# Kernel optimization log

Measured on AMD Instinct MI355X. Metric: run time of the kernel, lower is better.

The kernel has to match this reference:

```python
import jax, jax.numpy as jnp
import numpy as np

N, E, MUL = 50000, 400000, 32
SQ3 = float(np.sqrt(3.0))


def setup_inputs() -> dict:
    key = jax.random.key(0)
    ks = jax.random.split(key, 16)
    rn = lambda k, s: jax.random.normal(k, s, dtype=jnp.float32)
    return {
        "x": rn(ks[0], (N, 4 * MUL)),                       # 32x0e + 32x1o
        "node_attr": jnp.ones((N, 1), jnp.float32),          # 1x0e
        "edge_src": jax.random.randint(ks[1], (E,), 0, N),
        "edge_dst": jax.random.randint(ks[2], (E,), 0, N),
        "edge_sh": rn(ks[3], (E, 4)),                        # SH(lmax=1): 0e + 1o
        "edge_scalars": jax.random.uniform(ks[4], (E, 10), dtype=jnp.float32),
        "W_fc1": rn(ks[5], (10, 100)),
        "W_fc2": rn(ks[6], (100, 4 * MUL)),
        "W_sc0": rn(ks[7], (MUL, MUL)),
        "W_sc1": rn(ks[8], (MUL, MUL)),
        "W_l1_0": rn(ks[9], (MUL, MUL)),
        "W_l1_1": rn(ks[10], (MUL, MUL)),
        "W_l2_0": rn(ks[11], (2 * MUL, MUL)),
        "W_l2_1": rn(ks[12], (2 * MUL, MUL)),
        "W_alpha": rn(ks[13], (2 * MUL, 1)),
    }


def reference(x, node_attr, edge_src, edge_dst, edge_sh, edge_scalars,
              W_fc1, W_fc2, W_sc0, W_sc1, W_l1_0, W_l1_1, W_l2_0, W_l2_1, W_alpha):
    n = x.shape[0]
    x0 = x[:, :MUL]                       # [N, 32]  scalars (0e)
    x1 = x[:, MUL:].reshape(n, MUL, 3)    # [N, 32, 3] vectors (1o)
    a = node_attr                          # [N, 1]
    inv = 1.0 / np.sqrt(MUL)
    inv2 = 1.0 / np.sqrt(2 * MUL)

    # self-connection FCTP(x, attr) -> out irreps (attr is scalar -> per-l linear)
    sc0 = (x0 @ W_sc0) * inv * a
    sc1 = jnp.einsum('nuc,uv->nvc', x1, W_sc1) * inv * a[:, :, None]
    sc = jnp.concatenate([sc0, sc1.reshape(n, 3 * MUL)], axis=1)

    # lin1
    y0 = (x0 @ W_l1_0) * inv * a
    y1 = jnp.einsum('nuc,uv->nvc', x1, W_l1_1) * inv * a[:, :, None]

    # radial MLP -> per-edge tensor-product weights (4 uvu paths x MUL)
    h = jax.nn.silu(edge_scalars @ W_fc1 / np.sqrt(10.0))
    w = (h @ W_fc2) / np.sqrt(100.0)      # [E, 4*MUL]
    w00, w11 = w[:, :MUL], w[:, MUL:2 * MUL]
    w01, w10 = w[:, 2 * MUL:3 * MUL], w[:, 3 * MUL:]

    # gather at source nodes
    x0e = y0[edge_src]                    # [E, 32]
    x1e = y1[edge_src]                    # [E, 32, 3]
    sh0 = edge_sh[:, :1]                  # [E, 1]
    sh1 = edge_sh[:, 1:4]                 # [E, 3]

    # CG-structured 'uvu' paths
    m00 = w00 * x0e * sh0                                           # 0e x 0e -> 0e
    m11 = w11 * jnp.einsum('euc,ec->eu', x1e, sh1) / SQ3            # 1o x 1o -> 0e
    m01 = w01[:, :, None] * x0e[:, :, None] * sh1[:, None, :]       # 0e x 1o -> 1o
    m10 = w10[:, :, None] * x1e * sh0[:, :, None]                   # 1o x 0e -> 1o
    edge_feat = jnp.concatenate(
        [m00, m11, m01.reshape(-1, 3 * MUL), m10.reshape(-1, 3 * MUL)], axis=1)  # [E, 256]

    # scatter-mean to destination nodes
    sums = jax.ops.segment_sum(edge_feat, edge_dst, num_segments=n)
    cnt = jax.ops.segment_sum(jnp.ones((edge_feat.shape[0],), x.dtype), edge_dst, num_segments=n)
    mean = sums / jnp.maximum(cnt, 1.0)[:, None]                    # [N, 256]

    mid0 = mean[:, :2 * MUL]                                        # 64x0e
    mid1 = mean[:, 2 * MUL:].reshape(n, 2 * MUL, 3)                 # 64x1o

    alpha = (mid0 @ W_alpha) * inv2 * a                             # [N, 1]
    c0 = (mid0 @ W_l2_0) * inv2 * a
    c1 = jnp.einsum('nuc,uv->nvc', mid1, W_l2_1) * inv2 * a[:, :, None]
    conv = jnp.concatenate([c0, c1.reshape(n, 3 * MUL)], axis=1)

    # output mask of sc is all ones here -> alpha gating as in source
    return sc + alpha * conv
```

## Files before the change

kernel.cpp:

```cpp
#include <hip/hip_runtime.h>
#include <hip/hip_bf16.h>

#define MUL 32
#define SCAN_CH 1024

typedef _Float16 f16x8 __attribute__((ext_vector_type(8)));
typedef float f32x4 __attribute__((ext_vector_type(4)));

static __device__ __forceinline__ float silu_f(float z) {
    return z / (1.0f + __expf(-z));
}

__global__ __launch_bounds__(256) void node_pre_kernel(
    const float* __restrict__ x, const float* __restrict__ attr,
    const float* __restrict__ Wsc0, const float* __restrict__ Wsc1,
    const float* __restrict__ Wl10, const float* __restrict__ Wl11,
    float* __restrict__ sc_out, _Float16* __restrict__ y_out, int N)
{
    __shared__ float sX[4][128];
    const int tid = threadIdx.x;
    const int wid = tid >> 6, L = tid & 63;
    float* xs = sX[wid];
    const float inv = 0.17677669529663687f;

    const bool t0 = (L < 32);
    const int i1 = t0 ? 0 : (L - 32);
    const int v1 = i1 / 3, c1 = i1 - v1 * 3;
    const int i2 = L + 32;
    const int v2 = i2 / 3, c2 = i2 - v2 * 3;

    const int xb1 = t0 ? 0 : (32 + c1);
    const int xst1 = t0 ? 1 : 3;

    float wA[32], wB[32], wC[32], wD[32];
#pragma unroll
    for (int u = 0; u < 32; ++u) {
        wA[u] = t0 ? Wsc0[u * 32 + L] : Wsc1[u * 32 + v1];
        wB[u] = t0 ? Wl10[u * 32 + L] : Wl11[u * 32 + v1];
        wC[u] = Wsc1[u * 32 + v2];
        wD[u] = Wl11[u * 32 + v2];
    }

    const int stride = gridDim.x * 4;
    for (int n = blockIdx.x * 4 + wid; n < N; n += stride) {
        xs[L]      = x[(size_t)n * 128 + L];
        xs[64 + L] = x[(size_t)n * 128 + 64 + L];
        const float scale = inv * attr[n];
        float a0 = 0.f, a1 = 0.f, b0 = 0.f, b1 = 0.f;
#pragma unroll
        for (int u = 0; u < 32; ++u) {
            const float xv1 = xs[xb1 + u * xst1];
            const float xv2 = xs[32 + u * 3 + c2];
            a0 += xv1 * wA[u];
            a1 += xv1 * wB[u];
            b0 += xv2 * wC[u];
            b1 += xv2 * wD[u];
        }
        sc_out[(size_t)n * 128 + L]      = a0 * scale;
        sc_out[(size_t)n * 128 + 64 + L] = b0 * scale;
        y_out [(size_t)n * 128 + L]      = (_Float16)(a1 * scale);
        y_out [(size_t)n * 128 + 64 + L] = (_Float16)(b1 * scale);
    }
}

__global__ void hist_kernel(const int* __restrict__ edst, int* __restrict__ deg, int E)
{
    int i = blockIdx.x * blockDim.x + threadIdx.x;
    const int stride = gridDim.x * blockDim.x;
    for (; i < E; i += stride) atomicAdd(&deg[edst[i]], 1);
}

__global__ __launch_bounds__(256) void scanA_kernel(
    const int* __restrict__ deg, int* __restrict__ bsum, int N)
{
    __shared__ int red[256];
    const int t = threadIdx.x, b = blockIdx.x;
    const int base = b * SCAN_CH;
    int s = 0;
#pragma unroll
    for (int k = 0; k < 4; ++k) {
        const int idx = base + t + k * 256;
        if (idx < N) s += deg[idx];
    }
    red[t] = s;
    __syncthreads();
    for (int off = 128; off; off >>= 1) {
        if (t < off) red[t] += red[t + off];
        __syncthreads();
    }
    if (t == 0) bsum[b] = red[0];
}

__global__ __launch_bounds__(256) void scanB_kernel(
    const int* __restrict__ bsum, int* __restrict__ boff, int NB)
{
    __shared__ int s[256];
    const int t = threadIdx.x;
    const int v = (t < NB) ? bsum[t] : 0;
    s[t] = v;
    __syncthreads();
    for (int off = 1; off < 256; off <<= 1) {
        const int add = (t >= off) ? s[t - off] : 0;
        __syncthreads();
        s[t] += add;
        __syncthreads();
    }
    if (t < NB) boff[t] = s[t] - v;
}

__global__ __launch_bounds__(256) void scanC_kernel(
    const int* __restrict__ deg, const int* __restrict__ boff,
    int* __restrict__ row_ptr, int N)
{
    __shared__ int ts[256];
    const int t = threadIdx.x, b = blockIdx.x;
    const int base = b * SCAN_CH + t * 4;
    int d0 = 0, d1 = 0, d2 = 0, d3 = 0;
    if (base + 0 < N) d0 = deg[base + 0];
    if (base + 1 < N) d1 = deg[base + 1];
    if (base + 2 < N) d2 = deg[base + 2];
    if (base + 3 < N) d3 = deg[base + 3];
    const int tsum = d0 + d1 + d2 + d3;
    ts[t] = tsum;
    __syncthreads();
    for (int off = 1; off < 256; off <<= 1) {
        const int add = (t >= off) ? ts[t - off] : 0;
        __syncthreads();
        ts[t] += add;
        __syncthreads();
    }
    int run = boff[b] + ts[t] - tsum;
    if (base + 0 <= N) row_ptr[base + 0] = run;
    run += d0;
    if (base + 1 <= N) row_ptr[base + 1] = run;
    run += d1;
    if (base + 2 <= N) row_ptr[base + 2] = run;
    run += d2;
    if (base + 3 <= N) row_ptr[base + 3] = run;
}

__global__ void fill_kernel(
    const int* __restrict__ esrc, const int* __restrict__ edst,
    const float* __restrict__ esh,
    const int* __restrict__ row_ptr, int* __restrict__ cur,
    int* __restrict__ csr2edge, int* __restrict__ src_s, float4* __restrict__ sh_s,
    int E)
{
    int i = blockIdx.x * blockDim.x + threadIdx.x;
    const int stride = gridDim.x * blockDim.x;
    for (; i < E; i += stride) {
        const int d = edst[i];
        const int p = row_ptr[d] + atomicAdd(&cur[d], 1);
        csr2edge[p] = i;
        src_s[p] = esrc[i];
        sh_s[p] = *(const float4*)&esh[(size_t)i * 4];
    }
}

__global__ __launch_bounds__(512) void edge_w_kernel(
    const float* __restrict__ escal, const int* __restrict__ csr2edge,
    const float* __restrict__ Wfc1, const float* __restrict__ Wfc2,
    _Float16* __restrict__ w_s, int E)
{
    __shared__ _Float16 sW2T[128 * 128];
    __shared__ _Float16 sH[8][16 * 128];

    const int tid = threadIdx.x;
    const int wid = tid >> 6;
    const int l   = tid & 63;
    const int c16 = l & 15;
    const int kq  = l >> 4;

    _Float16* Hw = sH[wid];

    {
        int* z2 = (int*)sW2T;
        for (int i = tid; i < 128 * 128 / 2; i += 512) z2[i] = 0;
    }
    __syncthreads();
    for (int i = tid; i < 100 * 128; i += 512) {
        const int k = i >> 7, col = i & 127;
        sW2T[col * 128 + (k ^ ((col & 7) << 3))] = (_Float16)Wfc2[i];
    }

    f16x8 bW1[7];
#pragma unroll
    for (int cb = 0; cb < 7; ++cb) {
        const int col = cb * 16 + c16;
#pragma unroll
        for (int j = 0; j < 8; ++j) {
            const int k = kq * 8 + j;
            bW1[cb][j] = (k < 10 && col < 100) ? (_Float16)Wfc1[k * 100 + col]
                                               : (_Float16)0.f;
        }
    }
#pragma unroll
    for (int r = 0; r < 4; ++r) {
        const int row = kq * 4 + r;
        const int col = 112 + c16;
        Hw[row * 128 + (col ^ ((row & 7) << 3))] = (_Float16)0.f;
    }
    __syncthreads();

    const float inv_s10 = 0.31622776601683794f;

    const int gw = blockIdx.x * 8 + wid;
    const int nw = gridDim.x * 8;
    const int step = nw * 16;

    int base = gw * 16;
    f16x8 a1;
    {
        const int ge = base + c16;
        const int ee = (ge < E) ? csr2edge[ge] : 0;
#pragma unroll
        for (int j = 0; j < 8; ++j) {
            const int k = kq * 8 + j;
            a1[j] = (k < 10 && ge < E) ? (_Float16)escal[(size_t)ee * 10 + k]
                                       : (_Float16)0.f;
        }
    }

    for (; base < E; base += step) {
#pragma unroll
        for (int cb = 0; cb < 7; ++cb) {
            f32x4 z = {0.f, 0.f, 0.f, 0.f};
            z = __builtin_amdgcn_mfma_f32_16x16x32_f16(a1, bW1[cb], z, 0, 0, 0);
#pragma unroll
            for (int r = 0; r < 4; ++r) {
                const int row = kq * 4 + r;
                const int col = cb * 16 + c16;
                const float h = silu_f(z[r] * inv_s10) * 0.1f;
                Hw[row * 128 + (col ^ ((row & 7) << 3))] = (_Float16)h;
            }
        }

        f16x8 a1n;
        {
            const int ge = base + step + c16;
            const int ee = (ge < E) ? csr2edge[ge] : 0;
#pragma unroll
            for (int j = 0; j < 8; ++j) {
                const int k = kq * 8 + j;
                a1n[j] = (k < 10 && ge < E)
                         ? (_Float16)escal[(size_t)ee * 10 + k]
                         : (_Float16)0.f;
            }
        }

        f32x4 acc0 = {0.f,0.f,0.f,0.f}, acc1 = {0.f,0.f,0.f,0.f};
        f32x4 acc2 = {0.f,0.f,0.f,0.f}, acc3 = {0.f,0.f,0.f,0.f};
        f32x4 acc4 = {0.f,0.f,0.f,0.f}, acc5 = {0.f,0.f,0.f,0.f};
        f32x4 acc6 = {0.f,0.f,0.f,0.f}, acc7 = {0.f,0.f,0.f,0.f};
#pragma unroll
        for (int kk = 0; kk < 4; ++kk) {
            const f16x8 a2 = *(const f16x8*)&Hw[c16 * 128 +
                                ((kk * 32 + kq * 8) ^ ((c16 & 7) << 3))];
#define BFRAG(CB) (*(const f16x8*)&sW2T[((CB) * 16 + c16) * 128 + \
                       ((kk * 32 + kq * 8) ^ ((c16 & 7) << 3))])
            acc0 = __builtin_amdgcn_mfma_f32_16x16x32_f16(a2, BFRAG(0), acc0, 0, 0, 0);
            acc1 = __builtin_amdgcn_mfma_f32_16x16x32_f16(a2, BFRAG(1), acc1, 0, 0, 0);
            acc2 = __builtin_amdgcn_mfma_f32_16x16x32_f16(a2, BFRAG(2), acc2, 0, 0, 0);
            acc3 = __builtin_amdgcn_mfma_f32_16x16x32_f16(a2, BFRAG(3), acc3, 0, 0, 0);
            acc4 = __builtin_amdgcn_mfma_f32_16x16x32_f16(a2, BFRAG(4), acc4, 0, 0, 0);
            acc5 = __builtin_amdgcn_mfma_f32_16x16x32_f16(a2, BFRAG(5), acc5, 0, 0, 0);
            acc6 = __builtin_amdgcn_mfma_f32_16x16x32_f16(a2, BFRAG(6), acc6, 0, 0, 0);
            acc7 = __builtin_amdgcn_mfma_f32_16x16x32_f16(a2, BFRAG(7), acc7, 0, 0, 0);
#undef BFRAG
        }

#define STAGE_CB(CB, ACC)                                                     \
        {                                                                     \
            _Pragma("unroll")                                                 \
            for (int r = 0; r < 4; ++r) {                                     \
                const int row = kq * 4 + r;                                   \
                const int col = (CB) * 16 + c16;                              \
                Hw[row * 128 + (col ^ ((row & 7) << 3))] = (_Float16)(ACC)[r];\
            }                                                                 \
        }
        STAGE_CB(0, acc0) STAGE_CB(1, acc1) STAGE_CB(2, acc2) STAGE_CB(3, acc3)
        STAGE_CB(4, acc4) STAGE_CB(5, acc5) STAGE_CB(6, acc6) STAGE_CB(7, acc7)
#undef STAGE_CB

#pragma unroll
        for (int i = 0; i < 4; ++i) {
            const int e = i * 4 + (l >> 4);
            const int colb = (l & 15) * 8;
            const f16x8 v = *(const f16x8*)&Hw[e * 128 +
                                (colb ^ ((e & 7) << 3))];
            if (base + e < E)
                *(f16x8*)&w_s[(size_t)(base + e) * 128 + colb] = v;
        }

        a1 = a1n;
    }
}

__global__ __launch_bounds__(256) void gather_post_kernel(
    const _Float16* __restrict__ w_s, const int* __restrict__ src_s,
    const float4* __restrict__ sh_s, const int* __restrict__ row_ptr,
    const _Float16* __restrict__ y, const float* __restrict__ attr,
    const float* __restrict__ Wl20, const float* __restrict__ Wl21,
    const float* __restrict__ Walpha,
    float* __restrict__ out, int N)
{
    __shared__ float sW0[64 * 32];
    __shared__ float sW1[64 * 32];
    __shared__ float sWa[64];
    __shared__ float sMid[4][256];

    const int tid = threadIdx.x;
    for (int i = tid; i < 64 * 32; i += 256) {
        sW0[i] = Wl20[i];
        sW1[i] = Wl21[i];
    }
    if (tid < 64) sWa[tid] = Walpha[tid];
    __syncthreads();

    const int wid = tid >> 6;
    const int L   = tid & 63;
    const bool hi = (L >= 32);
    const int u   = L & 31;

    const int wAi = hi ? 32 + u : u;
    const int wBi = hi ? 96 + u : 64 + u;
    const int yi0 = hi ? 32 + 3 * u + 0 : u;
    const int yi1 = hi ? 32 + 3 * u + 1 : u;
    const int yi2 = hi ? 32 + 3 * u + 2 : u;
    const float mulA = hi ? 0.5773502691896258f : 1.0f;

    const int o1m = L - 32;
    const int v1 = hi ? o1m / 3 : 0;
    const int c1 = hi ? o1m - v1 * 3 : 0;
    const int o2m = L + 32;
    const int v2 = o2m / 3;
    const int c2 = o2m - v2 * 3;
    const float* wcol1 = hi ? (sW1 + v1) : (sW0 + L);
    const float* wcol2 = sW1 + v2;

    float* midw = &sMid[wid][0];
    const float* msrc1c = hi ? (midw + 64 + c1 * 64) : midw;
    const float* msrc2c = midw + 64 + c2 * 64;

#define ACC_EDGE(sh, wAv, wBv, q0, q1, q2) do {                        \
        const float sA0 = hi ? (sh).y : (sh).x;                        \
        const float sA1 = hi ? (sh).z : 0.f;                           \
        const float sA2 = hi ? (sh).w : 0.f;                           \
        const float b1s = hi ? (sh).x : (sh).y;                        \
        const float b2s = hi ? (sh).x : (sh).z;                        \
        const float b3s = hi ? (sh).x : (sh).w;                        \
        accA += (wAv) * mulA * ((q0) * sA0 + (q1) * sA1 + (q2) * sA2); \
        acc1 += (wBv) * (q0) * b1s;                                    \
        acc2 += (wBv) * (q1) * b2s;                                    \
        acc3 += (wBv) * (q2) * b3s;                                    \
    } while (0)

    const int waves_glob = gridDim.x * 4;
    for (int n = blockIdx.x * 4 + wid; n < N; n += waves_glob) {
        const int jlo = row_ptr[n];
        const int jhi = row_ptr[n + 1];
        const int deg = jhi - jlo;
        if (deg <= 0) continue;

        float accA = 0.f, acc1 = 0.f, acc2 = 0.f, acc3 = 0.f;

        int j = jlo;
        for (; j + 2 <= jhi; j += 2) {
            const int sa = src_s[j];
            const int sb = src_s[j + 1];
            const float4 shA = sh_s[j];
            const float4 shB = sh_s[j + 1];
            const _Float16* wra = w_s + (size_t)j * 128;
            const _Float16* wrb = wra + 128;
            const _Float16* yra = y + (size_t)sa * 128;
            const _Float16* yrb = y + (size_t)sb * 128;
            const float wAa = (float)wra[wAi], wBa = (float)wra[wBi];
            const float qa0 = (float)yra[yi0], qa1 = (float)yra[yi1], qa2 = (float)yra[yi2];
            const float wAb = (float)wrb[wAi], wBb = (float)wrb[wBi];
            const float qb0 = (float)yrb[yi0], qb1 = (float)yrb[yi1], qb2 = (float)yrb[yi2];
            ACC_EDGE(shA, wAa, wBa, qa0, qa1, qa2);
            ACC_EDGE(shB, wAb, wBb, qb0, qb1, qb2);
        }
        if (j < jhi) {
            const int sa = src_s[j];
            const float4 shA = sh_s[j];
            const _Float16* wra = w_s + (size_t)j * 128;
            const _Float16* yra = y + (size_t)sa * 128;
            const float wAa = (float)wra[wAi], wBa = (float)wra[wBi];
            const float qa0 = (float)yra[yi0], qa1 = (float)yra[yi1], qa2 = (float)yra[yi2];
            ACC_EDGE(shA, wAa, wBa, qa0, qa1, qa2);
        }

        const float rdeg = 1.0f / (float)deg;
        const float a = attr[n];

        float term = accA * rdeg * sWa[L];
#pragma unroll
        for (int off = 32; off; off >>= 1) term += __shfl_xor(term, off);
        const float alpha = term * 0.125f * a;

        midw[L]            = accA * rdeg;
        midw[64 + L]       = acc1 * rdeg;
        midw[128 + L]      = acc2 * rdeg;
        midw[192 + L]      = acc3 * rdeg;

        float cv1 = 0.f, cv2 = 0.f;
#pragma unroll
        for (int kk = 0; kk < 16; ++kk) {
            const float4 m1 = *(const float4*)&msrc1c[4 * kk];
            const float4 m2 = *(const float4*)&msrc2c[4 * kk];
            cv1 += m1.x * wcol1[(4 * kk + 0) * 32] + m1.y * wcol1[(4 * kk + 1) * 32]
                 + m1.z * wcol1[(4 * kk + 2) * 32] + m1.w * wcol1[(4 * kk + 3) * 32];
            cv2 += m2.x * wcol2[(4 * kk + 0) * 32] + m2.y * wcol2[(4 * kk + 1) * 32]
                 + m2.z * wcol2[(4 * kk + 2) * 32] + m2.w * wcol2[(4 * kk + 3) * 32];
        }
        const float f = alpha * 0.125f * a;
        const size_t ob = (size_t)n * 128;
        out[ob + L]      += f * cv1;
        out[ob + 64 + L] += f * cv2;
    }
#undef ACC_EDGE
}

extern "C" void kernel_launch(void* const* d_in, const int* in_sizes, int n_in,
                              void* d_out, int out_size, void* d_ws, size_t ws_size,
                              hipStream_t stream)
{
    const float* x      = (const float*)d_in[0];
    const float* attr   = (const float*)d_in[1];
    const int*   esrc   = (const int*)  d_in[2];
    const int*   edst   = (const int*)  d_in[3];
    const float* esh    = (const float*)d_in[4];
    const float* escal  = (const float*)d_in[5];
    const float* Wfc1   = (const float*)d_in[6];
    const float* Wfc2   = (const float*)d_in[7];
    const float* Wsc0   = (const float*)d_in[8];
    const float* Wsc1   = (const float*)d_in[9];
    const float* Wl10   = (const float*)d_in[10];
    const float* Wl11   = (const float*)d_in[11];
    const float* Wl20   = (const float*)d_in[12];
    const float* Wl21   = (const float*)d_in[13];
    const float* Walpha = (const float*)d_in[14];

    const int N = in_sizes[1];
    const int E = in_sizes[2];
    float* out = (float*)d_out;

    char* p = (char*)d_ws;
    _Float16* y   = (_Float16*)p; p += (size_t)N * 128 * sizeof(_Float16);
    int* row_ptr  = (int*)p;      p += (size_t)(N + 1) * sizeof(int);
    int* deg      = (int*)p;      p += (size_t)N * sizeof(int);
    int* cur      = (int*)p;      p += (size_t)N * sizeof(int);
    int* bsum     = (int*)p;      p += 256 * sizeof(int);
    int* boff     = (int*)p;      p += 256 * sizeof(int);
    int* csr2edge = (int*)p;      p += (size_t)E * sizeof(int);
    int* src_s    = (int*)p;      p += (size_t)E * sizeof(int);
    p = (char*)(((uintptr_t)p + 15) & ~(uintptr_t)15);
    float4* sh_s  = (float4*)p;   p += (size_t)E * sizeof(float4);
    _Float16* w_s = (_Float16*)p;

    const int NB = (N + SCAN_CH) / SCAN_CH;

    hipMemsetAsync(deg, 0, (size_t)2 * N * sizeof(int), stream);

    node_pre_kernel<<<1024, 256, 0, stream>>>(x, attr, Wsc0, Wsc1, Wl10, Wl11,
                                              out, y, N);
    hist_kernel<<<512, 256, 0, stream>>>(edst, deg, E);
    scanA_kernel<<<NB, 256, 0, stream>>>(deg, bsum, N);
    scanB_kernel<<<1, 256, 0, stream>>>(bsum, boff, NB);
    scanC_kernel<<<NB, 256, 0, stream>>>(deg, boff, row_ptr, N);
    fill_kernel<<<512, 256, 0, stream>>>(esrc, edst, esh, row_ptr, cur,
                                         csr2edge, src_s, sh_s, E);
    edge_w_kernel<<<512, 512, 0, stream>>>(escal, csr2edge, Wfc1, Wfc2, w_s, E);
    gather_post_kernel<<<4096, 256, 0, stream>>>(w_s, src_s, sh_s, row_ptr,
                                                 y, attr, Wl20, Wl21, Walpha,
                                                 out, N);
}
```

Measured before the change: 243.2 us.

## Fuse radial MLP edge weights with per-node gather-aggregation in one kernel

The edge-weight kernel now partitions the destination-sorted CSR edge range into contiguous per-wave spans aligned to node boundaries, found by binary search on row_ptr. Right after computing each 16-edge tile of tensor-product weights with MFMA, it consumes them from LDS to accumulate the message for each destination node. This removes the round trip of the per-edge weight array (E×128 fp16) through global memory. A small node_post kernel then reads a new fp16 per-node mean buffer and applies the output linears and alpha gating. In exchange, each wave walks its edges one at a time with dependent gathers of y, which reduces memory-level parallelism. The per-node means are also rounded to fp16.

```diff
diff --git a/kernel.cpp b/kernel.cpp
--- a/kernel.cpp
+++ b/kernel.cpp
@@ -9,6 +9,16 @@
 
 static __device__ __forceinline__ float silu_f(float z) {
     return z / (1.0f + __expf(-z));
+}
+
+static __device__ __forceinline__ int lbound(const int* __restrict__ rp,
+                                             int cnt, int target) {
+    int lo = 0, hi = cnt;
+    while (lo < hi) {
+        const int mid = (lo + hi) >> 1;
+        if (rp[mid] < target) lo = mid + 1; else hi = mid;
+    }
+    return lo;
 }
 
 __global__ __launch_bounds__(256) void node_pre_kernel(
@@ -157,10 +167,12 @@
     }
 }
 
-__global__ __launch_bounds__(512) void edge_w_kernel(
+__global__ __launch_bounds__(512) void edge_fused_kernel(
     const float* __restrict__ escal, const int* __restrict__ csr2edge,
     const float* __restrict__ Wfc1, const float* __restrict__ Wfc2,
-    _Float16* __restrict__ w_s, int E)
+    const int* __restrict__ src_s, const float4* __restrict__ sh_s,
+    const int* __restrict__ row_ptr, const _Float16* __restrict__ y,
+    _Float16* __restrict__ mid_g, int N, int E)
 {
     __shared__ _Float16 sW2T[128 * 128];
     __shared__ _Float16 sH[8][16 * 128];
@@ -203,25 +215,47 @@
     __syncthreads();
 
     const float inv_s10 = 0.31622776601683794f;
-
-    const int gw = blockIdx.x * 8 + wid;
-    const int nw = gridDim.x * 8;
-    const int step = nw * 16;
-
-    int base = gw * 16;
+    const float inv_s3  = 0.5773502691896258f;
+
+    const bool hi = (l >= 32);
+    const int u = l & 31;
+    const int wAi = hi ? 32 + u : u;
+    const int wBi = hi ? 96 + u : 64 + u;
+    const int yi0 = hi ? 32 + 3 * u + 0 : u;
+    const int yi1 = hi ? 32 + 3 * u + 1 : u;
+    const int yi2 = hi ? 32 + 3 * u + 2 : u;
+    const float mulA = hi ? inv_s3 : 1.0f;
+
+    const int W = gridDim.x * 8;
+    const int k_w = blockIdx.x * 8 + wid;
+    const int tgt0 = (int)((long)k_w * E / W);
+    const int tgt1 = (int)((long)(k_w + 1) * E / W);
+    const int nlo = lbound(row_ptr, N + 1, tgt0);
+    const int nhi = lbound(row_ptr, N + 1, tgt1);
+    if (nlo >= nhi) return;
+    const int jstart = row_ptr[nlo];
+    const int jend   = row_ptr[nhi];
+    if (jstart >= jend) return;
+
+    int n = nlo;
+    while (n < nhi && row_ptr[n + 1] == row_ptr[n]) ++n;
+    int jhi_n = row_ptr[n + 1];
+
+    float accA = 0.f, ac1 = 0.f, ac2 = 0.f, ac3 = 0.f;
+
     f16x8 a1;
     {
-        const int ge = base + c16;
-        const int ee = (ge < E) ? csr2edge[ge] : 0;
+        const int ge = jstart + c16;
+        const int ee = (ge < jend) ? csr2edge[ge] : 0;
 #pragma unroll
         for (int j = 0; j < 8; ++j) {
             const int k = kq * 8 + j;
-            a1[j] = (k < 10 && ge < E) ? (_Float16)escal[(size_t)ee * 10 + k]
-                                       : (_Float16)0.f;
-        }
-    }
-
-    for (; base < E; base += step) {
+            a1[j] = (k < 10 && ge < jend)
+                    ? (_Float16)escal[(size_t)ee * 10 + k] : (_Float16)0.f;
+        }
+    }
+
+    for (int bb = jstart; bb < jend; bb += 16) {
 #pragma unroll
         for (int cb = 0; cb < 7; ++cb) {
             f32x4 z = {0.f, 0.f, 0.f, 0.f};
@@ -237,35 +271,34 @@
 
         f16x8 a1n;
         {
-            const int ge = base + step + c16;
-            const int ee = (ge < E) ? csr2edge[ge] : 0;
+            const int ge = bb + 16 + c16;
+            const int ee = (ge < jend) ? csr2edge[ge] : 0;
 #pragma unroll
             for (int j = 0; j < 8; ++j) {
                 const int k = kq * 8 + j;
-                a1n[j] = (k < 10 && ge < E)
-                         ? (_Float16)escal[(size_t)ee * 10 + k]
-                         : (_Float16)0.f;
+                a1n[j] = (k < 10 && ge < jend)
+                         ? (_Float16)escal[(size_t)ee * 10 + k] : (_Float16)0.f;
             }
         }
 
-        f32x4 acc0 = {0.f,0.f,0.f,0.f}, acc1 = {0.f,0.f,0.f,0.f};
-        f32x4 acc2 = {0.f,0.f,0.f,0.f}, acc3 = {0.f,0.f,0.f,0.f};
-        f32x4 acc4 = {0.f,0.f,0.f,0.f}, acc5 = {0.f,0.f,0.f,0.f};
-        f32x4 acc6 = {0.f,0.f,0.f,0.f}, acc7 = {0.f,0.f,0.f,0.f};
+        f32x4 acw0 = {0.f,0.f,0.f,0.f}, acw1 = {0.f,0.f,0.f,0.f};
+        f32x4 acw2 = {0.f,0.f,0.f,0.f}, acw3 = {0.f,0.f,0.f,0.f};
+        f32x4 acw4 = {0.f,0.f,0.f,0.f}, acw5 = {0.f,0.f,0.f,0.f};
+        f32x4 acw6 = {0.f,0.f,0.f,0.f}, acw7 = {0.f,0.f,0.f,0.f};
 #pragma unroll
         for (int kk = 0; kk < 4; ++kk) {
             const f16x8 a2 = *(const f16x8*)&Hw[c16 * 128 +
                                 ((kk * 32 + kq * 8) ^ ((c16 & 7) << 3))];
 #define BFRAG(CB) (*(const f16x8*)&sW2T[((CB) * 16 + c16) * 128 + \
                        ((kk * 32 + kq * 8) ^ ((c16 & 7) << 3))])
-            acc0 = __builtin_amdgcn_mfma_f32_16x16x32_f16(a2, BFRAG(0), acc0, 0, 0, 0);
-            acc1 = __builtin_amdgcn_mfma_f32_16x16x32_f16(a2, BFRAG(1), acc1, 0, 0, 0);
-            acc2 = __builtin_amdgcn_mfma_f32_16x16x32_f16(a2, BFRAG(2), acc2, 0, 0, 0);
-            acc3 = __builtin_amdgcn_mfma_f32_16x16x32_f16(a2, BFRAG(3), acc3, 0, 0, 0);
-            acc4 = __builtin_amdgcn_mfma_f32_16x16x32_f16(a2, BFRAG(4), acc4, 0, 0, 0);
-            acc5 = __builtin_amdgcn_mfma_f32_16x16x32_f16(a2, BFRAG(5), acc5, 0, 0, 0);
-            acc6 = __builtin_amdgcn_mfma_f32_16x16x32_f16(a2, BFRAG(6), acc6, 0, 0, 0);
-            acc7 = __builtin_amdgcn_mfma_f32_16x16x32_f16(a2, BFRAG(7), acc7, 0, 0, 0);
+            acw0 = __builtin_amdgcn_mfma_f32_16x16x32_f16(a2, BFRAG(0), acw0, 0, 0, 0);
+            acw1 = __builtin_amdgcn_mfma_f32_16x16x32_f16(a2, BFRAG(1), acw1, 0, 0, 0);
+            acw2 = __builtin_amdgcn_mfma_f32_16x16x32_f16(a2, BFRAG(2), acw2, 0, 0, 0);
+            acw3 = __builtin_amdgcn_mfma_f32_16x16x32_f16(a2, BFRAG(3), acw3, 0, 0, 0);
+            acw4 = __builtin_amdgcn_mfma_f32_16x16x32_f16(a2, BFRAG(4), acw4, 0, 0, 0);
+            acw5 = __builtin_amdgcn_mfma_f32_16x16x32_f16(a2, BFRAG(5), acw5, 0, 0, 0);
+            acw6 = __builtin_amdgcn_mfma_f32_16x16x32_f16(a2, BFRAG(6), acw6, 0, 0, 0);
+            acw7 = __builtin_amdgcn_mfma_f32_16x16x32_f16(a2, BFRAG(7), acw7, 0, 0, 0);
 #undef BFRAG
         }
 
@@ -278,28 +311,55 @@
                 Hw[row * 128 + (col ^ ((row & 7) << 3))] = (_Float16)(ACC)[r];\
             }                                                                 \
         }
-        STAGE_CB(0, acc0) STAGE_CB(1, acc1) STAGE_CB(2, acc2) STAGE_CB(3, acc3)
-        STAGE_CB(4, acc4) STAGE_CB(5, acc5) STAGE_CB(6, acc6) STAGE_CB(7, acc7)
+        STAGE_CB(0, acw0) STAGE_CB(1, acw1) STAGE_CB(2, acw2) STAGE_CB(3, acw3)
+        STAGE_CB(4, acw4) STAGE_CB(5, acw5) STAGE_CB(6, acw6) STAGE_CB(7, acw7)
 #undef STAGE_CB
 
-#pragma unroll
-        for (int i = 0; i < 4; ++i) {
-            const int e = i * 4 + (l >> 4);
-            const int colb = (l & 15) * 8;
-            const f16x8 v = *(const f16x8*)&Hw[e * 128 +
-                                (colb ^ ((e & 7) << 3))];
-            if (base + e < E)
-                *(f16x8*)&w_s[(size_t)(base + e) * 128 + colb] = v;
+        const int nb = (jend - bb < 16) ? (jend - bb) : 16;
+        for (int e = 0; e < nb; ++e) {
+            const int jj = bb + e;
+            const int sa = src_s[jj];
+            const float4 sh = sh_s[jj];
+            const int sw = (e & 7) << 3;
+            const float wAv = (float)Hw[e * 128 + (wAi ^ sw)];
+            const float wBv = (float)Hw[e * 128 + (wBi ^ sw)];
+            const _Float16* yr = y + (size_t)sa * 128;
+            const float q0 = (float)yr[yi0];
+            const float q1 = (float)yr[yi1];
+            const float q2 = (float)yr[yi2];
+            const float sA0 = hi ? sh.y : sh.x;
+            const float sA1 = hi ? sh.z : 0.f;
+            const float sA2 = hi ? sh.w : 0.f;
+            const float b1s = hi ? sh.x : sh.y;
+            const float b2s = hi ? sh.x : sh.z;
+            const float b3s = hi ? sh.x : sh.w;
+            accA += wAv * mulA * (q0 * sA0 + q1 * sA1 + q2 * sA2);
+            ac1  += wBv * q0 * b1s;
+            ac2  += wBv * q1 * b2s;
+            ac3  += wBv * q2 * b3s;
+
+            if (jj + 1 == jhi_n) {
+                const int rlo = row_ptr[n];
+                const float rdeg = 1.0f / (float)(jhi_n - rlo);
+                _Float16* mg = mid_g + (size_t)n * 256;
+                mg[l]       = (_Float16)(accA * rdeg);
+                mg[64 + l]  = (_Float16)(ac1 * rdeg);
+                mg[128 + l] = (_Float16)(ac2 * rdeg);
+                mg[192 + l] = (_Float16)(ac3 * rdeg);
+                accA = ac1 = ac2 = ac3 = 0.f;
+                ++n;
+                while (n < nhi && row_ptr[n + 1] == row_ptr[n]) ++n;
+                if (n < nhi) jhi_n = row_ptr[n + 1];
+            }
         }
 
         a1 = a1n;
     }
 }
 
-__global__ __launch_bounds__(256) void gather_post_kernel(
-    const _Float16* __restrict__ w_s, const int* __restrict__ src_s,
-    const float4* __restrict__ sh_s, const int* __restrict__ row_ptr,
-    const _Float16* __restrict__ y, const float* __restrict__ attr,
+__global__ __launch_bounds__(256) void node_post_kernel(
+    const _Float16* __restrict__ mid_g, const int* __restrict__ row_ptr,
+    const float* __restrict__ attr,
     const float* __restrict__ Wl20, const float* __restrict__ Wl21,
     const float* __restrict__ Walpha,
     float* __restrict__ out, int N)
@@ -320,14 +380,6 @@
     const int wid = tid >> 6;
     const int L   = tid & 63;
     const bool hi = (L >= 32);
-    const int u   = L & 31;
-
-    const int wAi = hi ? 32 + u : u;
-    const int wBi = hi ? 96 + u : 64 + u;
-    const int yi0 = hi ? 32 + 3 * u + 0 : u;
-    const int yi1 = hi ? 32 + 3 * u + 1 : u;
-    const int yi2 = hi ? 32 + 3 * u + 2 : u;
-    const float mulA = hi ? 0.5773502691896258f : 1.0f;
 
     const int o1m = L - 32;
     const int v1 = hi ? o1m / 3 : 0;
@@ -342,84 +394,43 @@
     const float* msrc1c = hi ? (midw + 64 + c1 * 64) : midw;
     const float* msrc2c = midw + 64 + c2 * 64;
 
-#define ACC_EDGE(sh, wAv, wBv, q0, q1, q2) do {                        \
-        const float sA0 = hi ? (sh).y : (sh).x;                        \
-        const float sA1 = hi ? (sh).z : 0.f;                           \
-        const float sA2 = hi ? (sh).w : 0.f;                           \
-        const float b1s = hi ? (sh).x : (sh).y;                        \
-        const float b2s = hi ? (sh).x : (sh).z;                        \
-        const float b3s = hi ? (sh).x : (sh).w;                        \
-        accA += (wAv) * mulA * ((q0) * sA0 + (q1) * sA1 + (q2) * sA2); \
-        acc1 += (wBv) * (q0) * b1s;                                    \
-        acc2 += (wBv) * (q1) * b2s;                                    \
-        acc3 += (wBv) * (q2) * b3s;                                    \
-    } while (0)
-
     const int waves_glob = gridDim.x * 4;
     for (int n = blockIdx.x * 4 + wid; n < N; n += waves_glob) {
-        const int jlo = row_ptr[n];
-        const int jhi = row_ptr[n + 1];
-        const int deg = jhi - jlo;
+        const int deg = row_ptr[n + 1] - row_ptr[n];
         if (deg <= 0) continue;
 
-        float accA = 0.f, acc1 = 0.f, acc2 = 0.f, acc3 = 0.f;
-
-        int j = jlo;
-        for (; j + 2 <= jhi; j += 2) {
-            const int sa = src_s[j];
-            const int sb = src_s[j + 1];
-            const float4 shA = sh_s[j];
-            const float4 shB = sh_s[j + 1];
-            const _Float16* wra = w_s + (size_t)j * 128;
-            const _Float16* wrb = wra + 128;
-            const _Float16* yra = y + (size_t)sa * 128;
-            const _Float16* yrb = y + (size_t)sb * 128;
-            const float wAa = (float)wra[wAi], wBa = (float)wra[wBi];
-            const float qa0 = (float)yra[yi0], qa1 = (float)yra[yi1], qa2 = (float)yra[yi2];
-            const float wAb = (float)wrb[wAi], wBb = (float)wrb[wBi];
-            const float qb0 = (float)yrb[yi0], qb1 = (float)yrb[yi1], qb2 = (float)yrb[yi2];
-            ACC_EDGE(shA, wAa, wBa, qa0, qa1, qa2);
-            ACC_EDGE(shB, wAb, wBb, qb0, qb1, qb2);
-        }
-        if (j < jhi) {
-            const int sa = src_s[j];
-            const float4 shA = sh_s[j];
-            const _Float16* wra = w_s + (size_t)j * 128;
-            const _Float16* yra = y + (size_t)sa * 128;
-            const float wAa = (float)wra[wAi], wBa = (float)wra[wBi];
-            const float qa0 = (float)yra[yi0], qa1 = (float)yra[yi1], qa2 = (float)yra[yi2];
-            ACC_EDGE(shA, wAa, wBa, qa0, qa1, qa2);
-        }
-
-        const float rdeg = 1.0f / (float)deg;
+        const _Float16* mg = mid_g + (size_t)n * 256;
+        const float m0 = (float)mg[L];
+        const float m1 = (float)mg[64 + L];
+        const float m2 = (float)mg[128 + L];
+        const float m3 = (float)mg[192 + L];
         const float a = attr[n];
 
-        float term = accA * rdeg * sWa[L];
+        float term = m0 * sWa[L];
 #pragma unroll
         for (int off = 32; off; off >>= 1) term += __shfl_xor(term, off);
         const float alpha = term * 0.125f * a;
 
-        midw[L]            = accA * rdeg;
-        midw[64 + L]       = acc1 * rdeg;
-        midw[128 + L]      = acc2 * rdeg;
-        midw[192 + L]      = acc3 * rdeg;
+        midw[L]       = m0;
+        midw[64 + L]  = m1;
+        midw[128 + L] = m2;
+        midw[192 + L] = m3;
 
         float cv1 = 0.f, cv2 = 0.f;
 #pragma unroll
         for (int kk = 0; kk < 16; ++kk) {
-            const float4 m1 = *(const float4*)&msrc1c[4 * kk];
-            const float4 m2 = *(const float4*)&msrc2c[4 * kk];
-            cv1 += m1.x * wcol1[(4 * kk + 0) * 32] + m1.y * wcol1[(4 * kk + 1) * 32]
-                 + m1.z * wcol1[(4 * kk + 2) * 32] + m1.w * wcol1[(4 * kk + 3) * 32];
-            cv2 += m2.x * wcol2[(4 * kk + 0) * 32] + m2.y * wcol2[(4 * kk + 1) * 32]
-                 + m2.z * wcol2[(4 * kk + 2) * 32] + m2.w * wcol2[(4 * kk + 3) * 32];
+            const float4 mm1 = *(const float4*)&msrc1c[4 * kk];
+            const float4 mm2 = *(const float4*)&msrc2c[4 * kk];
+            cv1 += mm1.x * wcol1[(4 * kk + 0) * 32] + mm1.y * wcol1[(4 * kk + 1) * 32]
+                 + mm1.z * wcol1[(4 * kk + 2) * 32] + mm1.w * wcol1[(4 * kk + 3) * 32];
+            cv2 += mm2.x * wcol2[(4 * kk + 0) * 32] + mm2.y * wcol2[(4 * kk + 1) * 32]
+                 + mm2.z * wcol2[(4 * kk + 2) * 32] + mm2.w * wcol2[(4 * kk + 3) * 32];
         }
         const float f = alpha * 0.125f * a;
         const size_t ob = (size_t)n * 128;
         out[ob + L]      += f * cv1;
         out[ob + 64 + L] += f * cv2;
     }
-#undef ACC_EDGE
 }
 
 extern "C" void kernel_launch(void* const* d_in, const int* in_sizes, int n_in,
@@ -457,7 +468,7 @@
     int* src_s    = (int*)p;      p += (size_t)E * sizeof(int);
     p = (char*)(((uintptr_t)p + 15) & ~(uintptr_t)15);
     float4* sh_s  = (float4*)p;   p += (size_t)E * sizeof(float4);
-    _Float16* w_s = (_Float16*)p;
+    _Float16* mid_g = (_Float16*)p;
 
     const int NB = (N + SCAN_CH) / SCAN_CH;
 
@@ -471,8 +482,9 @@
     scanC_kernel<<<NB, 256, 0, stream>>>(deg, boff, row_ptr, N);
     fill_kernel<<<512, 256, 0, stream>>>(esrc, edst, esh, row_ptr, cur,
                                          csr2edge, src_s, sh_s, E);
-    edge_w_kernel<<<512, 512, 0, stream>>>(escal, csr2edge, Wfc1, Wfc2, w_s, E);
-    gather_post_kernel<<<4096, 256, 0, stream>>>(w_s, src_s, sh_s, row_ptr,
-                                                 y, attr, Wl20, Wl21, Walpha,
-                                                 out, N);
-}
+    edge_fused_kernel<<<512, 512, 0, stream>>>(escal, csr2edge, Wfc1, Wfc2,
+                                               src_s, sh_s, row_ptr, y,
+                                               mid_g, N, E);
+    node_post_kernel<<<1024, 256, 0, stream>>>(mid_g, row_ptr, attr,
+                                               Wl20, Wl21, Walpha, out, N);
+}
```

Result: slower. 383.5 us (+57.7%).
